# Kernel tuning notes

Hardware: AMD Instinct MI355X
Metric: run time of the kernel (lower is better)

## Reference

```python
import jax, jax.numpy as jnp
import numpy as np
import math

B, IN_DIM, HID, OUT_DIM = 8192, 64, 256, 4096
N_STEPS = 20


def logx_and_kl(loga, logb, alpha):
    # logx = log(alpha*a + (1-alpha)*b); kl = KL(x || b)
    logx = jnp.logaddexp(loga + jnp.log(alpha), logb + jnp.log(1.0 - alpha))
    kl = jnp.sum(jnp.exp(logx) * (logx - logb), axis=-1, keepdims=True)
    return logx, kl


def dkl_dalpha(loga, logb, logx):
    a_minus_b = jnp.exp(loga) - jnp.exp(logb)
    return jnp.sum(a_minus_b * (logx - logb + 1.0), axis=-1, keepdims=True)


def findalphafork(loga, logb, k, n_steps=N_STEPS):
    def body(i, carry):
        alpha, bot, top = carry
        logx, kl = logx_and_kl(loga, logb, alpha)
        bot = jnp.where(k >= kl, alpha, bot)
        top = jnp.where(k <= kl, alpha, top)
        d = dkl_dalpha(loga, logb, logx)
        delta = (k - kl) / (d + 1e-12)
        alpha = jnp.clip(alpha + delta,
                         bot * (15.0 / 16.0) + top * (1.0 / 16.0),
                         bot * 0.5 + top * 0.5)
        return alpha, bot, top

    init = (jnp.ones_like(k), jnp.zeros_like(k), jnp.ones_like(k))
    alpha, _, _ = jax.lax.fori_loop(0, n_steps, body, init)
    return alpha


def kl_fixed_mixture(k, loga, logb):
    alpha = findalphafork(loga, logb, k)
    return logx_and_kl(loga, logb, alpha)


def setup_inputs() -> dict:
    key = jax.random.key(0)
    ks = jax.random.split(key, 10)
    x = jax.random.normal(ks[0], (B, IN_DIM), dtype=jnp.float32)
    kl_budget = jax.random.uniform(ks[1], (B, 1), dtype=jnp.float32)
    log_base_dist = jax.nn.log_softmax(
        jax.random.normal(ks[2], (B, OUT_DIM), dtype=jnp.float32), axis=-1)
    W0 = jax.random.normal(ks[3], (HID, IN_DIM + 1), dtype=jnp.float32) * (0.05 / math.sqrt(IN_DIM + 1))
    b0 = jax.random.normal(ks[4], (HID,), dtype=jnp.float32) * 0.01
    W1 = jax.random.normal(ks[5], (HID, HID), dtype=jnp.float32) * (1.0 / math.sqrt(HID))
    b1 = jax.random.normal(ks[6], (HID,), dtype=jnp.float32) * 0.01
    W2 = jax.random.normal(ks[7], (OUT_DIM + 1, HID), dtype=jnp.float32) * 0.01
    b2 = jax.random.normal(ks[8], (OUT_DIM + 1,), dtype=jnp.float32) * 0.01
    return {"x": x, "kl_budget": kl_budget, "log_base_dist": log_base_dist,
            "W0": W0, "b0": b0, "W1": W1, "b1": b1, "W2": W2, "b2": b2,
            "actions_left": 16}


def reference(x, kl_budget, log_base_dist, W0, b0, W1, b1, W2, b2, actions_left):
    h = jnp.concatenate([x, kl_budget], axis=-1)  # [B, IN_DIM+1]
    for i, (W, b) in enumerate(((W0, b0), (W1, b1), (W2, b2))):
        if i != 0:
            h = jnp.tanh(h)
        h = h @ W.T + b
    # n_versions_last_layer == 1 -> selected_x = h
    kl_target = jax.nn.sigmoid(h[:, :1] - math.log(actions_left)) * kl_budget + 1e-6
    loga = h[:, 1:] + log_base_dist
    loga = loga - jnp.max(loga, axis=-1, keepdims=True)
    loga = loga - jax.nn.logsumexp(loga, axis=-1, keepdims=True)
    logx, kl_achieved = kl_fixed_mixture(kl_target, loga, log_base_dist)
    return jax.nn.softmax(logx, axis=-1), jnp.square(kl_achieved - kl_target)
```

## Files before the change

### kernel.cpp

```cpp
#include <hip/hip_runtime.h>
#include <hip/hip_bf16.h>
#include <math.h>

typedef float f32x4 __attribute__((ext_vector_type(4)));
typedef __bf16 bf16x8 __attribute__((ext_vector_type(8)));
typedef unsigned short ushort;

#define NROWS 8192
#define HID 256
#define NCOL 4096
#define NSTEPS 20

static __device__ inline float bf2f(ushort u) {
    union { unsigned int i; float f; } c; c.i = ((unsigned int)u) << 16; return c.f;
}
static __device__ inline ushort f2bf(float x) {
    __hip_bfloat16 h = __float2bfloat16(x);
    union { __hip_bfloat16 h; ushort u; } c; c.h = h; return c.u;
}
static __device__ inline void gload_lds16(const void* g, void* l) {
    __builtin_amdgcn_global_load_lds(
        (const __attribute__((address_space(1))) void*)g,
        (__attribute__((address_space(3))) void*)l, 16, 0, 0);
}

__global__ __launch_bounds__(256) void mlp01_kernel(
    const float* __restrict__ x, const float* __restrict__ klb,
    const float* __restrict__ W0, const float* __restrict__ b0,
    const float* __restrict__ W1, const float* __restrict__ b1,
    const float* __restrict__ W2, const float* __restrict__ b2,
    const int* __restrict__ AL,
    ushort* __restrict__ t_ext, float* __restrict__ kt)
{
    __shared__ float xk[8][66];
    __shared__ float h0[8][HID];
    __shared__ float ktred[8][4];
    const int tid = threadIdx.x;
    const int lane = tid & 63, w = tid >> 6;
    const int r0 = blockIdx.x * 8;

    for (int f = tid; f < 8 * 64; f += 256) {
        int r = f >> 6, k = f & 63;
        xk[r][k] = x[(r0 + r) * 64 + k];
    }
    if (tid < 8) xk[tid][64] = klb[r0 + tid];
    __syncthreads();

    {
        float acc[8];
        float bb = b0[tid];
        #pragma unroll
        for (int r = 0; r < 8; r++) acc[r] = bb;
        for (int k = 0; k < 65; k++) {
            float w0 = W0[tid * 65 + k];
            #pragma unroll
            for (int r = 0; r < 8; r++) acc[r] += w0 * xk[r][k];
        }
        #pragma unroll
        for (int r = 0; r < 8; r++) h0[r][tid] = tanhf(acc[r]);
    }
    __syncthreads();
    {
        float acc[8];
        float bb = b1[tid];
        #pragma unroll
        for (int r = 0; r < 8; r++) acc[r] = bb;
        for (int k = 0; k < HID; k++) {
            float w1 = W1[tid * HID + k];
            #pragma unroll
            for (int r = 0; r < 8; r++) acc[r] += w1 * h0[r][k];
        }
        const float w2v = W2[tid];
        __syncthreads();
        #pragma unroll
        for (int r = 0; r < 8; r++) {
            float v = tanhf(acc[r]);
            ushort hi = f2bf(v);
            float lo = v - bf2f(hi);
            size_t base = (size_t)(r0 + r) * 512;
            t_ext[base + tid] = hi;
            t_ext[base + 256 + tid] = f2bf(lo);
            float p = v * w2v;
            #pragma unroll
            for (int off = 1; off < 64; off <<= 1) p += __shfl_xor(p, off);
            if (lane == 0) ktred[r][w] = p;
        }
        __syncthreads();
        if (tid < 8) {
            float accv = ktred[tid][0] + ktred[tid][1] + ktred[tid][2] + ktred[tid][3];
            float z = accv + b2[0] - logf((float)AL[0]);
            float sg = 1.0f / (1.0f + expf(-z));
            kt[r0 + tid] = sg * klb[r0 + tid] + 1e-6f;
        }
    }
}

__global__ __launch_bounds__(256) void w2ext_kernel(const float* __restrict__ W2,
                                                    ushort* __restrict__ Bext)
{
    const int r = blockIdx.x, t = threadIdx.x;
    float v = W2[(size_t)(r + 1) * 256 + t];
    ushort hi = f2bf(v);
    float lo = v - bf2f(hi);
    Bext[(size_t)r * 512 + t] = hi;
    Bext[(size_t)r * 512 + 256 + t] = f2bf(lo);
}

__global__ __launch_bounds__(256) void gemm2_mfma(
    const ushort* __restrict__ Aext, const ushort* __restrict__ Bext,
    const float* __restrict__ b2, float* __restrict__ h2out)
{
    __shared__ ushort As[128 * 64];
    __shared__ ushort Bs[128 * 64];
    const int tid = threadIdx.x;
    const int lane = tid & 63, w = tid >> 6;
    const int m0 = blockIdx.y * 128, c0 = blockIdx.x * 128;
    const int wm = w & 1, wn = w >> 1;

    f32x4 acc[4][4];
    #pragma unroll
    for (int i = 0; i < 4; i++)
        #pragma unroll
        for (int j = 0; j < 4; j++) acc[i][j] = (f32x4){0.f, 0.f, 0.f, 0.f};

    int sg_row[4], sg_c[4];
    #pragma unroll
    for (int s = 0; s < 4; s++) {
        int idx = (s * 4 + w) * 512 + lane * 8;
        int row = idx >> 6;
        int cp = (idx >> 3) & 7;
        sg_row[s] = row;
        sg_c[s] = cp ^ (row & 7);
    }

    for (int kt = 0; kt < 8; kt++) {
        const int k0 = kt * 64;
        #pragma unroll
        for (int s = 0; s < 4; s++) {
            gload_lds16(&Aext[(size_t)(m0 + sg_row[s]) * 512 + k0 + sg_c[s] * 8],
                        &As[(s * 4 + w) * 512]);
            gload_lds16(&Bext[(size_t)(c0 + sg_row[s]) * 512 + k0 + sg_c[s] * 8],
                        &Bs[(s * 4 + w) * 512]);
        }
        __syncthreads();
        #pragma unroll
        for (int kk = 0; kk < 2; kk++) {
            const int cA = kk * 4 + (lane >> 4);
            bf16x8 af[4], bfr[4];
            #pragma unroll
            for (int i = 0; i < 4; i++) {
                int mr = wm * 64 + i * 16 + (lane & 15);
                af[i] = *(const bf16x8*)&As[mr * 64 + ((cA ^ (mr & 7)) * 8)];
                int nr = wn * 64 + i * 16 + (lane & 15);
                bfr[i] = *(const bf16x8*)&Bs[nr * 64 + ((cA ^ (nr & 7)) * 8)];
            }
            #pragma unroll
            for (int i = 0; i < 4; i++)
                #pragma unroll
                for (int j = 0; j < 4; j++)
                    acc[i][j] = __builtin_amdgcn_mfma_f32_16x16x32_bf16(
                        af[i], bfr[j], acc[i][j], 0, 0, 0);
        }
        __syncthreads();
    }

    const int colb = c0 + wn * 64 + (lane & 15);
    #pragma unroll
    for (int j = 0; j < 4; j++) {
        float bias = b2[1 + colb + j * 16];
        #pragma unroll
        for (int i = 0; i < 4; i++) {
            int rr = m0 + wm * 64 + i * 16 + (lane >> 4) * 4;
            #pragma unroll
            for (int q = 0; q < 4; q++)
                h2out[(size_t)(rr + q) * 4096 + colb + j * 16] = acc[i][j][q] + bias;
        }
    }
}

__global__ __launch_bounds__(256) void solve_kernel(
    float* __restrict__ outbuf, const float* __restrict__ logb_g,
    const float* __restrict__ ktarr)
{
    __shared__ float red[16];
    const int tid = threadIdx.x;
    const int lane = tid & 63, w = tid >> 6;
    const int r = blockIdx.x;

    const float* rowA = outbuf + (size_t)r * 4096;
    const float* rowB = logb_g + (size_t)r * 4096;

    f32x4 av4[4], bv4[4];
    #pragma unroll
    for (int c = 0; c < 4; c++) {
        av4[c] = *(const f32x4*)&rowA[c * 1024 + tid * 4];
        bv4[c] = *(const f32x4*)&rowB[c * 1024 + tid * 4];
    }

    float e[16];
    float s = 0.0f, sav = 0.0f;
    #pragma unroll
    for (int c = 0; c < 4; c++)
        #pragma unroll
        for (int j = 0; j < 4; j++) {
            int m = c * 4 + j;
            e[m] = __expf(av4[c][j] + bv4[c][j]);
            s += e[m];
            sav = fmaf(e[m], av4[c][j], sav);
        }
    #pragma unroll
    for (int off = 1; off < 64; off <<= 1) {
        s   += __shfl_xor(s, off);
        sav += __shfl_xor(sav, off);
    }
    if (lane == 0) { red[w * 2] = s; red[w * 2 + 1] = sav; }
    __syncthreads();
    s   = red[0] + red[2] + red[4] + red[6];
    sav = red[1] + red[3] + red[5] + red[7];

    const float k = ktarr[r];
    const float lns = __logf(s);
    const float inv = 1.0f / s;
    const float kl1 = fmaf(sav, inv, -lns);

    float* orow = outbuf + (size_t)r * 4096;

    if (k >= kl1) {
        #pragma unroll
        for (int c = 0; c < 4; c++) {
            f32x4 o;
            #pragma unroll
            for (int j = 0; j < 4; j++) o[j] = e[c * 4 + j] * inv;
            *(f32x4*)&orow[c * 1024 + tid * 4] = o;
        }
        if (tid == 0) {
            float d = kl1 - k;
            outbuf[(size_t)NROWS * NCOL + r] = d * d;
        }
        return;
    }

    float eb[16];
    float c2 = 0.0f, c3 = 0.0f, seb = 0.0f, samv = 0.0f;
    #pragma unroll
    for (int c = 0; c < 4; c++)
        #pragma unroll
        for (int j = 0; j < 4; j++) {
            int m = c * 4 + j;
            float b = __expf(bv4[c][j]);
            eb[m] = b;
            float a = fmaf(e[m], inv, -b);
            e[m] = a;
            c2  = fmaf(b, bv4[c][j], c2);
            c3  = fmaf(a, bv4[c][j], c3);
            seb += b;
            samv = fmaf(a, av4[c][j], samv);
        }
    #pragma unroll
    for (int off = 1; off < 64; off <<= 1) {
        c2   += __shfl_xor(c2, off);
        c3   += __shfl_xor(c3, off);
        seb  += __shfl_xor(seb, off);
        samv += __shfl_xor(samv, off);
    }
    __syncthreads();
    if (lane == 0) {
        red[w * 4 + 0] = c2;  red[w * 4 + 1] = c3;
        red[w * 4 + 2] = seb; red[w * 4 + 3] = samv;
    }
    __syncthreads();
    c2   = red[0] + red[4] + red[8]  + red[12];
    c3   = red[1] + red[5] + red[9]  + red[13];
    seb  = red[2] + red[6] + red[10] + red[14];
    samv = red[3] + red[7] + red[11] + red[15];

    const float C2 = c2;
    const float C3 = c3;
    const float C4 = (1.0f - seb) - C3;

    float skl = kl1, a_eval = 1.0f;
    float bot = 0.0f, top = 1.0f;
    float d1 = samv - lns * (1.0f - seb) + C4;
    float alpha = fminf(0.5f, fmaxf(1.0f / 16.0f,
                        1.0f + (k - kl1) / (d1 + 1e-12f)));

    for (int it = 1; it < NSTEPS; it++) {
        a_eval = alpha;
        float kacc = 0.0f, dacc = 0.0f;
        #pragma unroll
        for (int m = 0; m < 16; m++) {
            float xv = fmaf(alpha, e[m], eb[m]);
            float lx = __logf(xv);
            kacc = fmaf(xv, lx, kacc);
            dacc = fmaf(e[m], lx, dacc);
        }
        #pragma unroll
        for (int off = 1; off < 64; off <<= 1) {
            kacc += __shfl_xor(kacc, off);
            dacc += __shfl_xor(dacc, off);
        }
        __syncthreads();
        if (lane == 0) { red[w * 2 + 0] = kacc; red[w * 2 + 1] = dacc; }
        __syncthreads();
        kacc = red[0] + red[2] + red[4] + red[6];
        dacc = red[1] + red[3] + red[5] + red[7];

        float klc = kacc - C2 - alpha * C3;
        float dc  = dacc + C4;
        skl = klc;

        bot = (k >= klc) ? alpha : bot;
        top = (k <= klc) ? alpha : top;
        float delta = (k - klc) / (dc + 1e-12f);
        float lo = bot * (15.0f / 16.0f) + top * (1.0f / 16.0f);
        float hi = 0.5f * (bot + top);
        alpha = fminf(hi, fmaxf(lo, alpha + delta));
        if (top - bot < 1e-6f) break;
    }

    if (alpha != a_eval) {
        float kacc = 0.0f;
        #pragma unroll
        for (int m = 0; m < 16; m++) {
            float xv = fmaf(alpha, e[m], eb[m]);
            kacc = fmaf(xv, __logf(xv), kacc);
        }
        #pragma unroll
        for (int off = 1; off < 64; off <<= 1) kacc += __shfl_xor(kacc, off);
        __syncthreads();
        if (lane == 0) red[w] = kacc;
        __syncthreads();
        kacc = red[0] + red[1] + red[2] + red[3];
        skl = kacc - C2 - alpha * C3;
    }

    const float spx = fmaf(alpha, 1.0f - seb, seb);
    const float invs = 1.0f / spx;

    #pragma unroll
    for (int c = 0; c < 4; c++) {
        f32x4 o;
        #pragma unroll
        for (int j = 0; j < 4; j++)
            o[j] = fmaf(alpha, e[c * 4 + j], eb[c * 4 + j]) * invs;
        *(f32x4*)&orow[c * 1024 + tid * 4] = o;
    }
    if (tid == 0) {
        float d = skl - k;
        outbuf[(size_t)NROWS * NCOL + r] = d * d;
    }
}

extern "C" void kernel_launch(void* const* d_in, const int* in_sizes, int n_in,
                              void* d_out, int out_size, void* d_ws, size_t ws_size,
                              hipStream_t stream)
{
    const float* x    = (const float*)d_in[0];
    const float* klb  = (const float*)d_in[1];
    const float* logb = (const float*)d_in[2];
    const float* W0   = (const float*)d_in[3];
    const float* b0   = (const float*)d_in[4];
    const float* W1   = (const float*)d_in[5];
    const float* b1   = (const float*)d_in[6];
    const float* W2   = (const float*)d_in[7];
    const float* b2   = (const float*)d_in[8];
    const int*   AL   = (const int*)d_in[9];
    float* out = (float*)d_out;

    ushort* tws  = (ushort*)d_ws;
    ushort* Bext = tws + (size_t)8192 * 512;
    float*  kt   = (float*)(Bext + (size_t)4096 * 512);

    hipLaunchKernelGGL(mlp01_kernel, dim3(1024), dim3(256), 0, stream,
                       x, klb, W0, b0, W1, b1, W2, b2, AL, tws, kt);
    hipLaunchKernelGGL(w2ext_kernel, dim3(4096), dim3(256), 0, stream, W2, Bext);
    hipLaunchKernelGGL(gemm2_mfma, dim3(32, 64), dim3(256), 0, stream, tws, Bext, b2, out);
    hipLaunchKernelGGL(solve_kernel, dim3(8192), dim3(256), 0, stream, out, logb, kt);
}
```

Baseline: 181.9 us.

## Fuse logsumexp partials into GEMM epilogue and store logits as fp16

The GEMM epilogue now adds log_base_dist, writes the combined logits as fp16 to a workspace buffer, and emits per-row partial sums of exp and exp*a for each column tile. The solve kernel then reduces those 32 partials instead of recomputing the first pass, and reads half-size fp16 logits rather than fp32 GEMM output. The aim is to cut the first reduction pass and HBM traffic between the two kernels. In exchange the GEMM reads logb with a strided, uncoalesced pattern, the non-converged path reads logb a second time, and fp16 storage of the logits loses precision. The path needs a large workspace, and the old kernels remain as a fallback.

```diff
diff --git a/kernel.cpp b/kernel.cpp
--- a/kernel.cpp
+++ b/kernel.cpp
@@ -4,6 +4,8 @@
 
 typedef float f32x4 __attribute__((ext_vector_type(4)));
 typedef __bf16 bf16x8 __attribute__((ext_vector_type(8)));
+typedef _Float16 f16;
+typedef _Float16 f16x4 __attribute__((ext_vector_type(4)));
 typedef unsigned short ushort;
 
 #define NROWS 8192
@@ -106,6 +108,276 @@
     Bext[(size_t)r * 512 + 256 + t] = f2bf(lo);
 }
 
+__global__ __launch_bounds__(256) void gemm2_fused(
+    const ushort* __restrict__ Aext, const ushort* __restrict__ Bext,
+    const float* __restrict__ b2, const float* __restrict__ logb,
+    f16* __restrict__ laraw, float2* __restrict__ partials)
+{
+    __shared__ ushort As[128 * 64];
+    __shared__ ushort Bs[128 * 64];
+    __shared__ float predls[2][128][2];
+    const int tid = threadIdx.x;
+    const int lane = tid & 63, w = tid >> 6;
+    const int m0 = blockIdx.y * 128, c0 = blockIdx.x * 128;
+    const int wm = w & 1, wn = w >> 1;
+
+    f32x4 acc[4][4];
+    #pragma unroll
+    for (int i = 0; i < 4; i++)
+        #pragma unroll
+        for (int j = 0; j < 4; j++) acc[i][j] = (f32x4){0.f, 0.f, 0.f, 0.f};
+
+    int sg_row[4], sg_c[4];
+    #pragma unroll
+    for (int s = 0; s < 4; s++) {
+        int idx = (s * 4 + w) * 512 + lane * 8;
+        int row = idx >> 6;
+        int cp = (idx >> 3) & 7;
+        sg_row[s] = row;
+        sg_c[s] = cp ^ (row & 7);
+    }
+
+    for (int kt = 0; kt < 8; kt++) {
+        const int k0 = kt * 64;
+        #pragma unroll
+        for (int s = 0; s < 4; s++) {
+            gload_lds16(&Aext[(size_t)(m0 + sg_row[s]) * 512 + k0 + sg_c[s] * 8],
+                        &As[(s * 4 + w) * 512]);
+            gload_lds16(&Bext[(size_t)(c0 + sg_row[s]) * 512 + k0 + sg_c[s] * 8],
+                        &Bs[(s * 4 + w) * 512]);
+        }
+        __syncthreads();
+        #pragma unroll
+        for (int kk = 0; kk < 2; kk++) {
+            const int cA = kk * 4 + (lane >> 4);
+            bf16x8 af[4], bfr[4];
+            #pragma unroll
+            for (int i = 0; i < 4; i++) {
+                int mr = wm * 64 + i * 16 + (lane & 15);
+                af[i] = *(const bf16x8*)&As[mr * 64 + ((cA ^ (mr & 7)) * 8)];
+                int nr = wn * 64 + i * 16 + (lane & 15);
+                bfr[i] = *(const bf16x8*)&Bs[nr * 64 + ((cA ^ (nr & 7)) * 8)];
+            }
+            #pragma unroll
+            for (int i = 0; i < 4; i++)
+                #pragma unroll
+                for (int j = 0; j < 4; j++)
+                    acc[i][j] = __builtin_amdgcn_mfma_f32_16x16x32_bf16(
+                        af[i], bfr[j], acc[i][j], 0, 0, 0);
+        }
+        __syncthreads();
+    }
+
+    const int colb = c0 + wn * 64 + (lane & 15);
+    const int rsub = (lane >> 4) * 4;
+    float pe[4][4], pav[4][4];
+    #pragma unroll
+    for (int i = 0; i < 4; i++)
+        #pragma unroll
+        for (int q = 0; q < 4; q++) { pe[i][q] = 0.0f; pav[i][q] = 0.0f; }
+
+    #pragma unroll
+    for (int j = 0; j < 4; j++) {
+        const int cg = colb + j * 16;
+        const float bias = b2[1 + cg];
+        #pragma unroll
+        for (int i = 0; i < 4; i++) {
+            #pragma unroll
+            for (int q = 0; q < 4; q++) {
+                const int rg = m0 + wm * 64 + i * 16 + rsub + q;
+                float av = acc[i][j][q] + bias;
+                float bv = logb[(size_t)rg * 4096 + cg];
+                float lr = av + bv;
+                laraw[(size_t)rg * 4096 + cg] = (f16)lr;
+                float e = __expf(lr);
+                pe[i][q] += e;
+                pav[i][q] = fmaf(e, av, pav[i][q]);
+            }
+        }
+    }
+    #pragma unroll
+    for (int mask = 1; mask < 16; mask <<= 1) {
+        #pragma unroll
+        for (int i = 0; i < 4; i++)
+            #pragma unroll
+            for (int q = 0; q < 4; q++) {
+                pe[i][q]  += __shfl_xor(pe[i][q], mask);
+                pav[i][q] += __shfl_xor(pav[i][q], mask);
+            }
+    }
+    if ((lane & 15) == 0) {
+        #pragma unroll
+        for (int i = 0; i < 4; i++)
+            #pragma unroll
+            for (int q = 0; q < 4; q++) {
+                int rl = wm * 64 + i * 16 + rsub + q;
+                predls[wn][rl][0] = pe[i][q];
+                predls[wn][rl][1] = pav[i][q];
+            }
+    }
+    __syncthreads();
+    if (tid < 128) {
+        float2 pp;
+        pp.x = predls[0][tid][0] + predls[1][tid][0];
+        pp.y = predls[0][tid][1] + predls[1][tid][1];
+        partials[(size_t)(m0 + tid) * 32 + blockIdx.x] = pp;
+    }
+}
+
+__global__ __launch_bounds__(256) void solve_fused(
+    float* __restrict__ out, const f16* __restrict__ laraw,
+    const float2* __restrict__ partials, const float* __restrict__ logb,
+    const float* __restrict__ ktarr)
+{
+    __shared__ float red[16];
+    const int tid = threadIdx.x;
+    const int lane = tid & 63, w = tid >> 6;
+    const int r = blockIdx.x;
+
+    float2 pv = partials[(size_t)r * 32 + (lane & 31)];
+    float s = pv.x, sav = pv.y;
+    #pragma unroll
+    for (int off = 1; off < 32; off <<= 1) {
+        s   += __shfl_xor(s, off);
+        sav += __shfl_xor(sav, off);
+    }
+    const float k = ktarr[r];
+    const float lns = __logf(s);
+    const float inv = 1.0f / s;
+    const float kl1 = fmaf(sav, inv, -lns);
+
+    const f16* lrow = laraw + (size_t)r * 4096;
+    float* orow = out + (size_t)r * 4096;
+
+    if (k >= kl1) {
+        #pragma unroll
+        for (int c = 0; c < 4; c++) {
+            f16x4 h4 = *(const f16x4*)&lrow[c * 1024 + tid * 4];
+            f32x4 o;
+            #pragma unroll
+            for (int j = 0; j < 4; j++) o[j] = __expf((float)h4[j]) * inv;
+            *(f32x4*)&orow[c * 1024 + tid * 4] = o;
+        }
+        if (tid == 0) {
+            float d = kl1 - k;
+            out[(size_t)NROWS * NCOL + r] = d * d;
+        }
+        return;
+    }
+
+    float am[16], eb[16];
+    float c2 = 0.0f, c3 = 0.0f, seb = 0.0f, samv = 0.0f;
+    #pragma unroll
+    for (int c = 0; c < 4; c++) {
+        f16x4 h4 = *(const f16x4*)&lrow[c * 1024 + tid * 4];
+        f32x4 b4 = *(const f32x4*)&logb[(size_t)r * 4096 + c * 1024 + tid * 4];
+        #pragma unroll
+        for (int j = 0; j < 4; j++) {
+            int m = c * 4 + j;
+            float lr = (float)h4[j], b = b4[j];
+            float e = __expf(lr);
+            float ebv = __expf(b);
+            float a = fmaf(e, inv, -ebv);
+            am[m] = a; eb[m] = ebv;
+            c2 = fmaf(ebv, b, c2);
+            c3 = fmaf(a, b, c3);
+            seb += ebv;
+            samv = fmaf(a, lr - b, samv);
+        }
+    }
+    #pragma unroll
+    for (int off = 1; off < 64; off <<= 1) {
+        c2   += __shfl_xor(c2, off);
+        c3   += __shfl_xor(c3, off);
+        seb  += __shfl_xor(seb, off);
+        samv += __shfl_xor(samv, off);
+    }
+    if (lane == 0) {
+        red[w * 4 + 0] = c2;  red[w * 4 + 1] = c3;
+        red[w * 4 + 2] = seb; red[w * 4 + 3] = samv;
+    }
+    __syncthreads();
+    c2   = red[0] + red[4] + red[8]  + red[12];
+    c3   = red[1] + red[5] + red[9]  + red[13];
+    seb  = red[2] + red[6] + red[10] + red[14];
+    samv = red[3] + red[7] + red[11] + red[15];
+
+    const float C2 = c2;
+    const float C3 = c3;
+    const float C4 = (1.0f - seb) - C3;
+
+    float skl = kl1, a_eval = 1.0f;
+    float bot = 0.0f, top = 1.0f;
+    float d1 = samv - lns * (1.0f - seb) + C4;
+    float alpha = fminf(0.5f, fmaxf(1.0f / 16.0f,
+                        1.0f + (k - kl1) / (d1 + 1e-12f)));
+
+    for (int it = 1; it < NSTEPS; it++) {
+        a_eval = alpha;
+        float kacc = 0.0f, dacc = 0.0f;
+        #pragma unroll
+        for (int m = 0; m < 16; m++) {
+            float xv = fmaf(alpha, am[m], eb[m]);
+            float lx = __logf(xv);
+            kacc = fmaf(xv, lx, kacc);
+            dacc = fmaf(am[m], lx, dacc);
+        }
+        #pragma unroll
+        for (int off = 1; off < 64; off <<= 1) {
+            kacc += __shfl_xor(kacc, off);
+            dacc += __shfl_xor(dacc, off);
+        }
+        __syncthreads();
+        if (lane == 0) { red[w * 2 + 0] = kacc; red[w * 2 + 1] = dacc; }
+        __syncthreads();
+        kacc = red[0] + red[2] + red[4] + red[6];
+        dacc = red[1] + red[3] + red[5] + red[7];
+
+        float klc = kacc - C2 - alpha * C3;
+        float dc  = dacc + C4;
+        skl = klc;
+
+        bot = (k >= klc) ? alpha : bot;
+        top = (k <= klc) ? alpha : top;
+        float delta = (k - klc) / (dc + 1e-12f);
+        float lo = bot * (15.0f / 16.0f) + top * (1.0f / 16.0f);
+        float hi = 0.5f * (bot + top);
+        alpha = fminf(hi, fmaxf(lo, alpha + delta));
+        if (top - bot < 1e-6f) break;
+    }
+
+    if (alpha != a_eval) {
+        float kacc = 0.0f;
+        #pragma unroll
+        for (int m = 0; m < 16; m++) {
+            float xv = fmaf(alpha, am[m], eb[m]);
+            kacc = fmaf(xv, __logf(xv), kacc);
+        }
+        #pragma unroll
+        for (int off = 1; off < 64; off <<= 1) kacc += __shfl_xor(kacc, off);
+        __syncthreads();
+        if (lane == 0) red[w] = kacc;
+        __syncthreads();
+        kacc = red[0] + red[1] + red[2] + red[3];
+        skl = kacc - C2 - alpha * C3;
+    }
+
+    const float spx = fmaf(alpha, 1.0f - seb, seb);
+    const float invs = 1.0f / spx;
+    #pragma unroll
+    for (int c = 0; c < 4; c++) {
+        f32x4 o;
+        #pragma unroll
+        for (int j = 0; j < 4; j++)
+            o[j] = fmaf(alpha, am[c * 4 + j], eb[c * 4 + j]) * invs;
+        *(f32x4*)&orow[c * 1024 + tid * 4] = o;
+    }
+    if (tid == 0) {
+        float d = skl - k;
+        out[(size_t)NROWS * NCOL + r] = d * d;
+    }
+}
+
 __global__ __launch_bounds__(256) void gemm2_mfma(
     const ushort* __restrict__ Aext, const ushort* __restrict__ Bext,
     const float* __restrict__ b2, float* __restrict__ h2out)
@@ -132,7 +404,6 @@
         sg_row[s] = row;
         sg_c[s] = cp ^ (row & 7);
     }
-
     for (int kt = 0; kt < 8; kt++) {
         const int k0 = kt * 64;
         #pragma unroll
@@ -163,7 +434,6 @@
         }
         __syncthreads();
     }
-
     const int colb = c0 + wn * 64 + (lane & 15);
     #pragma unroll
     for (int j = 0; j < 4; j++) {
@@ -196,7 +466,6 @@
         av4[c] = *(const f32x4*)&rowA[c * 1024 + tid * 4];
         bv4[c] = *(const f32x4*)&rowB[c * 1024 + tid * 4];
     }
-
     float e[16];
     float s = 0.0f, sav = 0.0f;
     #pragma unroll
@@ -222,7 +491,6 @@
     const float lns = __logf(s);
     const float inv = 1.0f / s;
     const float kl1 = fmaf(sav, inv, -lns);
-
     float* orow = outbuf + (size_t)r * 4096;
 
     if (k >= kl1) {
@@ -239,7 +507,6 @@
         }
         return;
     }
-
     float eb[16];
     float c2 = 0.0f, c3 = 0.0f, seb = 0.0f, samv = 0.0f;
     #pragma unroll
@@ -274,16 +541,13 @@
     seb  = red[2] + red[6] + red[10] + red[14];
     samv = red[3] + red[7] + red[11] + red[15];
 
-    const float C2 = c2;
-    const float C3 = c3;
+    const float C2 = c2, C3 = c3;
     const float C4 = (1.0f - seb) - C3;
-
     float skl = kl1, a_eval = 1.0f;
     float bot = 0.0f, top = 1.0f;
     float d1 = samv - lns * (1.0f - seb) + C4;
     float alpha = fminf(0.5f, fmaxf(1.0f / 16.0f,
                         1.0f + (k - kl1) / (d1 + 1e-12f)));
-
     for (int it = 1; it < NSTEPS; it++) {
         a_eval = alpha;
         float kacc = 0.0f, dacc = 0.0f;
@@ -304,11 +568,9 @@
         __syncthreads();
         kacc = red[0] + red[2] + red[4] + red[6];
         dacc = red[1] + red[3] + red[5] + red[7];
-
         float klc = kacc - C2 - alpha * C3;
         float dc  = dacc + C4;
         skl = klc;
-
         bot = (k >= klc) ? alpha : bot;
         top = (k <= klc) ? alpha : top;
         float delta = (k - klc) / (dc + 1e-12f);
@@ -317,7 +579,6 @@
         alpha = fminf(hi, fmaxf(lo, alpha + delta));
         if (top - bot < 1e-6f) break;
     }
-
     if (alpha != a_eval) {
         float kacc = 0.0f;
         #pragma unroll
@@ -333,10 +594,8 @@
         kacc = red[0] + red[1] + red[2] + red[3];
         skl = kacc - C2 - alpha * C3;
     }
-
     const float spx = fmaf(alpha, 1.0f - seb, seb);
     const float invs = 1.0f / spx;
-
     #pragma unroll
     for (int c = 0; c < 4; c++) {
         f32x4 o;
@@ -367,13 +626,28 @@
     const int*   AL   = (const int*)d_in[9];
     float* out = (float*)d_out;
 
-    ushort* tws  = (ushort*)d_ws;
-    ushort* Bext = tws + (size_t)8192 * 512;
-    float*  kt   = (float*)(Bext + (size_t)4096 * 512);
+    const size_t MB = 1048576ull;
+    char* p = (char*)d_ws;
+    ushort* tws   = (ushort*)(p);
+    ushort* Bext  = (ushort*)(p + 8 * MB);
+    float*  kt    = (float*) (p + 12 * MB);
+    f16*    laraw = (f16*)   (p + 16 * MB);
+    float2* part  = (float2*)(p + 80 * MB);
+    const size_t NEED = 82 * MB;
 
     hipLaunchKernelGGL(mlp01_kernel, dim3(1024), dim3(256), 0, stream,
                        x, klb, W0, b0, W1, b1, W2, b2, AL, tws, kt);
     hipLaunchKernelGGL(w2ext_kernel, dim3(4096), dim3(256), 0, stream, W2, Bext);
-    hipLaunchKernelGGL(gemm2_mfma, dim3(32, 64), dim3(256), 0, stream, tws, Bext, b2, out);
-    hipLaunchKernelGGL(solve_kernel, dim3(8192), dim3(256), 0, stream, out, logb, kt);
-}
+
+    if (ws_size >= NEED) {
+        hipLaunchKernelGGL(gemm2_fused, dim3(32, 64), dim3(256), 0, stream,
+                           tws, Bext, b2, logb, laraw, part);
+        hipLaunchKernelGGL(solve_fused, dim3(8192), dim3(256), 0, stream,
+                           out, laraw, part, logb, kt);
+    } else {
+        hipLaunchKernelGGL(gemm2_mfma, dim3(32, 64), dim3(256), 0, stream,
+                           tws, Bext, b2, out);
+        hipLaunchKernelGGL(solve_kernel, dim3(8192), dim3(256), 0, stream,
+                           out, logb, kt);
+    }
+}
```

Measured after the change: 190.8 us. +4.9%, slower.

## Store GEMM logits as fp16 workspace and solve rows with 512-thread blocks

Applied to the files above, without the earlier changes.

The output-layer GEMM now writes its logits in fp16 to a separate workspace instead of fp32 into the output buffer, which halves the intermediate write and read traffic between the GEMM and the solver. The solver now uses 512 threads per row with 8 elements each, which lowers register pressure and raises occupancy. tanhf is replaced by an exp-based fast tanh, and the bias is pre-copied to an aligned buffer. Rounding the logits to fp16 adds precision loss in the softmax/KL inputs, and the 8-wave reduction adds a few more LDS reads per iteration.

```diff
diff --git a/kernel.cpp b/kernel.cpp
--- a/kernel.cpp
+++ b/kernel.cpp
@@ -4,6 +4,8 @@
 
 typedef float f32x4 __attribute__((ext_vector_type(4)));
 typedef __bf16 bf16x8 __attribute__((ext_vector_type(8)));
+typedef _Float16 f16;
+typedef _Float16 f16x8 __attribute__((ext_vector_type(8)));
 typedef unsigned short ushort;
 
 #define NROWS 8192
@@ -17,6 +19,10 @@
 static __device__ inline ushort f2bf(float x) {
     __hip_bfloat16 h = __float2bfloat16(x);
     union { __hip_bfloat16 h; ushort u; } c; c.h = h; return c.u;
+}
+static __device__ inline float fast_tanh(float x) {
+    float e = __expf(2.0f * x);
+    return 1.0f - 2.0f / (e + 1.0f);
 }
 static __device__ inline void gload_lds16(const void* g, void* l) {
     __builtin_amdgcn_global_load_lds(
@@ -57,7 +63,7 @@
             for (int r = 0; r < 8; r++) acc[r] += w0 * xk[r][k];
         }
         #pragma unroll
-        for (int r = 0; r < 8; r++) h0[r][tid] = tanhf(acc[r]);
+        for (int r = 0; r < 8; r++) h0[r][tid] = fast_tanh(acc[r]);
     }
     __syncthreads();
     {
@@ -74,7 +80,7 @@
         __syncthreads();
         #pragma unroll
         for (int r = 0; r < 8; r++) {
-            float v = tanhf(acc[r]);
+            float v = fast_tanh(acc[r]);
             ushort hi = f2bf(v);
             float lo = v - bf2f(hi);
             size_t base = (size_t)(r0 + r) * 512;
@@ -96,7 +102,9 @@
 }
 
 __global__ __launch_bounds__(256) void w2ext_kernel(const float* __restrict__ W2,
-                                                    ushort* __restrict__ Bext)
+                                                    const float* __restrict__ b2,
+                                                    ushort* __restrict__ Bext,
+                                                    float* __restrict__ b2s)
 {
     const int r = blockIdx.x, t = threadIdx.x;
     float v = W2[(size_t)(r + 1) * 256 + t];
@@ -104,11 +112,12 @@
     float lo = v - bf2f(hi);
     Bext[(size_t)r * 512 + t] = hi;
     Bext[(size_t)r * 512 + 256 + t] = f2bf(lo);
+    if (t == 0) b2s[r] = b2[r + 1];
 }
 
 __global__ __launch_bounds__(256) void gemm2_mfma(
     const ushort* __restrict__ Aext, const ushort* __restrict__ Bext,
-    const float* __restrict__ b2, float* __restrict__ h2out)
+    const float* __restrict__ b2s, f16* __restrict__ h2f)
 {
     __shared__ ushort As[128 * 64];
     __shared__ ushort Bs[128 * 64];
@@ -167,47 +176,43 @@
     const int colb = c0 + wn * 64 + (lane & 15);
     #pragma unroll
     for (int j = 0; j < 4; j++) {
-        float bias = b2[1 + colb + j * 16];
+        float bias = b2s[colb + j * 16];
         #pragma unroll
         for (int i = 0; i < 4; i++) {
             int rr = m0 + wm * 64 + i * 16 + (lane >> 4) * 4;
             #pragma unroll
             for (int q = 0; q < 4; q++)
-                h2out[(size_t)(rr + q) * 4096 + colb + j * 16] = acc[i][j][q] + bias;
-        }
-    }
-}
-
-__global__ __launch_bounds__(256) void solve_kernel(
-    float* __restrict__ outbuf, const float* __restrict__ logb_g,
-    const float* __restrict__ ktarr)
-{
-    __shared__ float red[16];
+                h2f[(size_t)(rr + q) * 4096 + colb + j * 16] = (f16)(acc[i][j][q] + bias);
+        }
+    }
+}
+
+__global__ __launch_bounds__(512) void solve512(
+    float* __restrict__ out, const f16* __restrict__ h2f,
+    const float* __restrict__ logb, const float* __restrict__ ktarr)
+{
+    __shared__ float red[32];
     const int tid = threadIdx.x;
     const int lane = tid & 63, w = tid >> 6;
     const int r = blockIdx.x;
 
-    const float* rowA = outbuf + (size_t)r * 4096;
-    const float* rowB = logb_g + (size_t)r * 4096;
-
-    f32x4 av4[4], bv4[4];
-    #pragma unroll
-    for (int c = 0; c < 4; c++) {
-        av4[c] = *(const f32x4*)&rowA[c * 1024 + tid * 4];
-        bv4[c] = *(const f32x4*)&rowB[c * 1024 + tid * 4];
-    }
-
-    float e[16];
+    const f16* hrow = h2f + (size_t)r * 4096;
+    const float* brow = logb + (size_t)r * 4096;
+
+    f16x8 h8 = *(const f16x8*)&hrow[tid * 8];
+    f32x4 bq0 = *(const f32x4*)&brow[tid * 8];
+    f32x4 bq1 = *(const f32x4*)&brow[tid * 8 + 4];
+
+    float av[8], bv[8], e[8];
     float s = 0.0f, sav = 0.0f;
     #pragma unroll
-    for (int c = 0; c < 4; c++)
-        #pragma unroll
-        for (int j = 0; j < 4; j++) {
-            int m = c * 4 + j;
-            e[m] = __expf(av4[c][j] + bv4[c][j]);
-            s += e[m];
-            sav = fmaf(e[m], av4[c][j], sav);
-        }
+    for (int j = 0; j < 8; j++) {
+        av[j] = (float)h8[j];
+        bv[j] = (j < 4) ? bq0[j & 3] : bq1[j & 3];
+        e[j] = __expf(av[j] + bv[j]);
+        s += e[j];
+        sav = fmaf(e[j], av[j], sav);
+    }
     #pragma unroll
     for (int off = 1; off < 64; off <<= 1) {
         s   += __shfl_xor(s, off);
@@ -215,47 +220,43 @@
     }
     if (lane == 0) { red[w * 2] = s; red[w * 2 + 1] = sav; }
     __syncthreads();
-    s   = red[0] + red[2] + red[4] + red[6];
-    sav = red[1] + red[3] + red[5] + red[7];
+    s = 0.0f; sav = 0.0f;
+    #pragma unroll
+    for (int i = 0; i < 8; i++) { s += red[i * 2]; sav += red[i * 2 + 1]; }
 
     const float k = ktarr[r];
     const float lns = __logf(s);
     const float inv = 1.0f / s;
     const float kl1 = fmaf(sav, inv, -lns);
 
-    float* orow = outbuf + (size_t)r * 4096;
+    float* orow = out + (size_t)r * 4096;
 
     if (k >= kl1) {
-        #pragma unroll
-        for (int c = 0; c < 4; c++) {
-            f32x4 o;
-            #pragma unroll
-            for (int j = 0; j < 4; j++) o[j] = e[c * 4 + j] * inv;
-            *(f32x4*)&orow[c * 1024 + tid * 4] = o;
-        }
+        f32x4 o0, o1;
+        #pragma unroll
+        for (int j = 0; j < 4; j++) { o0[j] = e[j] * inv; o1[j] = e[j + 4] * inv; }
+        *(f32x4*)&orow[tid * 8] = o0;
+        *(f32x4*)&orow[tid * 8 + 4] = o1;
         if (tid == 0) {
             float d = kl1 - k;
-            outbuf[(size_t)NROWS * NCOL + r] = d * d;
+            out[(size_t)NROWS * NCOL + r] = d * d;
         }
         return;
     }
 
-    float eb[16];
+    float am[8], eb[8];
     float c2 = 0.0f, c3 = 0.0f, seb = 0.0f, samv = 0.0f;
     #pragma unroll
-    for (int c = 0; c < 4; c++)
-        #pragma unroll
-        for (int j = 0; j < 4; j++) {
-            int m = c * 4 + j;
-            float b = __expf(bv4[c][j]);
-            eb[m] = b;
-            float a = fmaf(e[m], inv, -b);
-            e[m] = a;
-            c2  = fmaf(b, bv4[c][j], c2);
-            c3  = fmaf(a, bv4[c][j], c3);
-            seb += b;
-            samv = fmaf(a, av4[c][j], samv);
-        }
+    for (int j = 0; j < 8; j++) {
+        float b = __expf(bv[j]);
+        eb[j] = b;
+        float a = fmaf(e[j], inv, -b);
+        am[j] = a;
+        c2   = fmaf(b, bv[j], c2);
+        c3   = fmaf(a, bv[j], c3);
+        seb += b;
+        samv = fmaf(a, av[j], samv);
+    }
     #pragma unroll
     for (int off = 1; off < 64; off <<= 1) {
         c2   += __shfl_xor(c2, off);
@@ -269,10 +270,14 @@
         red[w * 4 + 2] = seb; red[w * 4 + 3] = samv;
     }
     __syncthreads();
-    c2   = red[0] + red[4] + red[8]  + red[12];
-    c3   = red[1] + red[5] + red[9]  + red[13];
-    seb  = red[2] + red[6] + red[10] + red[14];
-    samv = red[3] + red[7] + red[11] + red[15];
+    c2 = 0.0f; c3 = 0.0f; seb = 0.0f; samv = 0.0f;
+    #pragma unroll
+    for (int i = 0; i < 8; i++) {
+        c2   += red[i * 4 + 0];
+        c3   += red[i * 4 + 1];
+        seb  += red[i * 4 + 2];
+        samv += red[i * 4 + 3];
+    }
 
     const float C2 = c2;
     const float C3 = c3;
@@ -280,7 +285,7 @@
 
     float skl = kl1, a_eval = 1.0f;
     float bot = 0.0f, top = 1.0f;
-    float d1 = samv - lns * (1.0f - seb) + C4;
+    float d1 = samv - lns * (1.0f - seb) + (1.0f - seb);
     float alpha = fminf(0.5f, fmaxf(1.0f / 16.0f,
                         1.0f + (k - kl1) / (d1 + 1e-12f)));
 
@@ -288,11 +293,11 @@
         a_eval = alpha;
         float kacc = 0.0f, dacc = 0.0f;
         #pragma unroll
-        for (int m = 0; m < 16; m++) {
-            float xv = fmaf(alpha, e[m], eb[m]);
+        for (int j = 0; j < 8; j++) {
+            float xv = fmaf(alpha, am[j], eb[j]);
             float lx = __logf(xv);
             kacc = fmaf(xv, lx, kacc);
-            dacc = fmaf(e[m], lx, dacc);
+            dacc = fmaf(am[j], lx, dacc);
         }
         #pragma unroll
         for (int off = 1; off < 64; off <<= 1) {
@@ -302,8 +307,9 @@
         __syncthreads();
         if (lane == 0) { red[w * 2 + 0] = kacc; red[w * 2 + 1] = dacc; }
         __syncthreads();
-        kacc = red[0] + red[2] + red[4] + red[6];
-        dacc = red[1] + red[3] + red[5] + red[7];
+        kacc = 0.0f; dacc = 0.0f;
+        #pragma unroll
+        for (int i = 0; i < 8; i++) { kacc += red[i * 2]; dacc += red[i * 2 + 1]; }
 
         float klc = kacc - C2 - alpha * C3;
         float dc  = dacc + C4;
@@ -321,8 +327,8 @@
     if (alpha != a_eval) {
         float kacc = 0.0f;
         #pragma unroll
-        for (int m = 0; m < 16; m++) {
-            float xv = fmaf(alpha, e[m], eb[m]);
+        for (int j = 0; j < 8; j++) {
+            float xv = fmaf(alpha, am[j], eb[j]);
             kacc = fmaf(xv, __logf(xv), kacc);
         }
         #pragma unroll
@@ -330,24 +336,25 @@
         __syncthreads();
         if (lane == 0) red[w] = kacc;
         __syncthreads();
-        kacc = red[0] + red[1] + red[2] + red[3];
+        kacc = 0.0f;
+        #pragma unroll
+        for (int i = 0; i < 8; i++) kacc += red[i];
         skl = kacc - C2 - alpha * C3;
     }
 
     const float spx = fmaf(alpha, 1.0f - seb, seb);
     const float invs = 1.0f / spx;
-
-    #pragma unroll
-    for (int c = 0; c < 4; c++) {
-        f32x4 o;
-        #pragma unroll
-        for (int j = 0; j < 4; j++)
-            o[j] = fmaf(alpha, e[c * 4 + j], eb[c * 4 + j]) * invs;
-        *(f32x4*)&orow[c * 1024 + tid * 4] = o;
-    }
+    f32x4 o0, o1;
+    #pragma unroll
+    for (int j = 0; j < 4; j++) {
+        o0[j] = fmaf(alpha, am[j], eb[j]) * invs;
+        o1[j] = fmaf(alpha, am[j + 4], eb[j + 4]) * invs;
+    }
+    *(f32x4*)&orow[tid * 8] = o0;
+    *(f32x4*)&orow[tid * 8 + 4] = o1;
     if (tid == 0) {
         float d = skl - k;
-        outbuf[(size_t)NROWS * NCOL + r] = d * d;
+        out[(size_t)NROWS * NCOL + r] = d * d;
     }
 }
 
@@ -367,13 +374,17 @@
     const int*   AL   = (const int*)d_in[9];
     float* out = (float*)d_out;
 
-    ushort* tws  = (ushort*)d_ws;
-    ushort* Bext = tws + (size_t)8192 * 512;
-    float*  kt   = (float*)(Bext + (size_t)4096 * 512);
+    const size_t MB = 1048576ull;
+    char* p = (char*)d_ws;
+    ushort* tws  = (ushort*)(p);
+    ushort* Bext = (ushort*)(p + 8 * MB);
+    float*  kt   = (float*) (p + 12 * MB);
+    float*  b2s  = (float*) (p + 12 * MB + 65536);
+    f16*    h2f  = (f16*)   (p + 16 * MB);
 
     hipLaunchKernelGGL(mlp01_kernel, dim3(1024), dim3(256), 0, stream,
                        x, klb, W0, b0, W1, b1, W2, b2, AL, tws, kt);
-    hipLaunchKernelGGL(w2ext_kernel, dim3(4096), dim3(256), 0, stream, W2, Bext);
-    hipLaunchKernelGGL(gemm2_mfma, dim3(32, 64), dim3(256), 0, stream, tws, Bext, b2, out);
-    hipLaunchKernelGGL(solve_kernel, dim3(8192), dim3(256), 0, stream, out, logb, kt);
-}
+    hipLaunchKernelGGL(w2ext_kernel, dim3(4096), dim3(256), 0, stream, W2, b2, Bext, b2s);
+    hipLaunchKernelGGL(gemm2_mfma, dim3(32, 64), dim3(256), 0, stream, tws, Bext, b2s, h2f);
+    hipLaunchKernelGGL(solve512, dim3(8192), dim3(512), 0, stream, out, h2f, logb, kt);
+}
```

After: 172.8 us. -5.0%, faster.
